# Kernel optimization log

Measured on AMD Instinct MI355X. Metric: run time of the kernel, lower is better.

## Reference

```python
import jax, jax.numpy as jnp
import numpy as np

N_NODES = 50000
N_EDGES = 800000
NODE_F = 5
EDGE_F = 4
HID = 128


def _glorot(key, shape):
    fan_in, fan_out = shape[0], shape[1]
    lim = float(np.sqrt(6.0 / (fan_in + fan_out)))
    return jax.random.uniform(key, shape, jnp.float32, -lim, lim)


def setup_inputs() -> dict:
    key = jax.random.key(0)
    ks = jax.random.split(key, 12)
    x = jax.random.normal(ks[0], (N_NODES, NODE_F), jnp.float32)
    edge_attr = jax.random.normal(ks[1], (N_EDGES, EDGE_F), jnp.float32)
    edge_index = jax.random.randint(ks[2], (2, N_EDGES), 0, N_NODES, jnp.int64)
    return {
        "x": x,
        "edge_attr": edge_attr,
        "W1": _glorot(ks[3], (NODE_F, HID)),
        "b1": jnp.zeros((HID,), jnp.float32),
        "W2": _glorot(ks[4], (HID, HID)),
        "b2": jnp.zeros((HID,), jnp.float32),
        "Wm1": _glorot(ks[5], (2 * HID + EDGE_F, HID)),
        "bm1": jnp.zeros((HID,), jnp.float32),
        "Wm2": _glorot(ks[6], (HID, 1)),
        "bm2": jnp.zeros((1,), jnp.float32),
        "edge_index": edge_index,
    }


def _gcn_conv(x, W, b, row, col, norm, n_nodes):
    # GCNConv: out = D^{-1/2} (A + I) D^{-1/2} X W + b
    xw = x @ W                                   # [N, H]
    msg = norm[:, None] * xw[row]                # [E+N, H] gather + scale
    agg = jax.ops.segment_sum(msg, col, num_segments=n_nodes)
    return agg + b


def reference(x, edge_attr, W1, b1, W2, b2, Wm1, bm1, Wm2, bm2, edge_index):
    n = x.shape[0]
    src, dst = edge_index[0], edge_index[1]
    # add self-loops (PyG GCNConv default)
    loop = jnp.arange(n, dtype=edge_index.dtype)
    row = jnp.concatenate([src, loop])
    col = jnp.concatenate([dst, loop])
    # symmetric normalization, in-degree w/ self-loops
    deg = jax.ops.segment_sum(jnp.ones_like(col, dtype=x.dtype), col, num_segments=n)
    dis = jnp.where(deg > 0, jax.lax.rsqrt(deg), 0.0)
    norm = dis[row] * dis[col]

    h = jax.nn.relu(_gcn_conv(x, W1, b1, row, col, norm, n))
    h = _gcn_conv(h, W2, b2, row, col, norm, n)

    # gather-concat edge MLP
    edge_emb = jnp.concatenate([h[src], h[dst], edge_attr], axis=1)  # [E, 2H+F]
    out = jax.nn.relu(edge_emb @ Wm1 + bm1) @ Wm2 + bm2              # [E, 1]
    return jax.nn.sigmoid(out[:, 0])
```

## Files before the change

### kernel.cpp

```cpp
#include <hip/hip_runtime.h>
#include <math.h>

#define HID 128
typedef unsigned int uint;
typedef __attribute__((ext_vector_type(8))) __bf16 bf16x8;
typedef __attribute__((ext_vector_type(4))) float f32x4;
typedef __attribute__((ext_vector_type(2))) float f32x2;


__device__ __forceinline__ uint pack_bf2(float x, float y) {
    union { float f; uint u; } a, b;
    a.f = x; b.f = y;
    uint lo = (a.u + 0x7fffu + ((a.u >> 16) & 1u)) >> 16;
    uint hi = (b.u + 0x7fffu + ((b.u >> 16) & 1u)) & 0xffff0000u;
    return lo | hi;
}

__device__ __forceinline__ unsigned short bf16r(float x) {
    union { float f; uint u; } a; a.f = x;
    return (unsigned short)((a.u + 0x7fffu + ((a.u >> 16) & 1u)) >> 16);
}

__device__ __forceinline__ f32x2 bf2f(uint v) {
    union { uint u[2]; f32x2 f; } r;
    r.u[0] = v << 16;
    r.u[1] = v & 0xffff0000u;
    return r.f;
}

__device__ __forceinline__ f32x2 mk2(float s) { f32x2 r; r.x = s; r.y = s; return r; }
__device__ __forceinline__ f32x2 max2z(f32x2 a) {
    f32x2 r; r.x = fmaxf(a.x, 0.f); r.y = fmaxf(a.y, 0.f); return r;
}

template<int CTRL>
__device__ __forceinline__ float dpp_add(float x) {
    union { float f; int i; } u, r;
    u.f = x;
    r.i = __builtin_amdgcn_update_dpp(0, u.i, CTRL, 0xf, 0xf, true);
    return x + r.f;
}


__global__ void prep_kernel(const float* __restrict__ W2, const float* __restrict__ Wm1,
                            const float* __restrict__ b2, const float* __restrict__ bm1,
                            uint* __restrict__ fWc, float* __restrict__ brow) {
    int t0 = blockIdx.x * blockDim.x + threadIdx.x;
    if (t0 < 65536) {
        int ks = t0 & 3;
        int i = t0 >> 2;
        int p = i & 3, lane = (i >> 2) & 63, kk = (i >> 8) & 3, ct = i >> 10;
        int k = kk * 32 + (lane >> 4) * 8 + p * 2;
        int n2 = ct * 16 + (lane & 15);
        const float* wmc = (n2 < 128) ? (Wm1 + n2) : (Wm1 + 128 * HID + (n2 - 128));
        const float* w2r0 = W2 + (size_t)k * HID + ks * 32;
        const float* w2r1 = w2r0 + HID;
        const float* wm = wmc + (size_t)(ks * 32) * HID;
        float d0 = 0.f, d1 = 0.f;
        #pragma unroll 8
        for (int j = 0; j < 32; ++j) {
            float w = wm[(size_t)j * HID];
            d0 += w2r0[j] * w;
            d1 += w2r1[j] * w;
        }
        d0 = dpp_add<0xB1>(d0); d0 = dpp_add<0x4E>(d0);
        d1 = dpp_add<0xB1>(d1); d1 = dpp_add<0x4E>(d1);
        if (ks == 0) fWc[i] = pack_bf2(d0, d1);
    } else if (t0 < 65536 + 1024) {
        int r = t0 - 65536;
        int ks = r & 3;
        int i = r >> 2;
        const float* wmc = (i < 128) ? (Wm1 + i) : (Wm1 + 128 * HID + (i - 128));
        float d = 0.f;
        for (int j = ks * 32; j < ks * 32 + 32; ++j) d += b2[j] * wmc[(size_t)j * HID];
        d = dpp_add<0xB1>(d); d = dpp_add<0x4E>(d);
        if (ks == 0) brow[i] = d + ((i < 128) ? bm1[i] : 0.f);
    }
}

__global__ void hist_rank(const int* __restrict__ dst, int* __restrict__ cnt,
                          int* __restrict__ rank, int E) {
    int e = blockIdx.x * blockDim.x + threadIdx.x;
    if (e < E) rank[e] = atomicAdd(&cnt[dst[e]], 1);
}

__global__ void scan1(const int* __restrict__ cnt, int* __restrict__ excl,
                      int* __restrict__ bsum, int N) {
    __shared__ int sh[256];
    int tid = threadIdx.x;
    int gid = blockIdx.x * 256 + tid;
    int v = (gid < N) ? cnt[gid] : 0;
    sh[tid] = v;
    __syncthreads();
    for (int o = 1; o < 256; o <<= 1) {
        int t = (tid >= o) ? sh[tid - o] : 0;
        __syncthreads();
        sh[tid] += t;
        __syncthreads();
    }
    if (gid < N) excl[gid] = sh[tid] - v;
    if (tid == 255) bsum[blockIdx.x] = sh[255];
}

__global__ void scan3x(const int* __restrict__ cnt, int* __restrict__ rowptr,
                       const int* __restrict__ bsum,
                       float* __restrict__ dis, const float* __restrict__ x,
                       uint4* __restrict__ xps, int N, int E, int NB) {
    __shared__ int sh[256];
    __shared__ int ex[256];
    int tid = threadIdx.x;
    int v = (tid < NB) ? bsum[tid] : 0;
    sh[tid] = v;
    __syncthreads();
    for (int o = 1; o < 256; o <<= 1) {
        int t = (tid >= o) ? sh[tid - o] : 0;
        __syncthreads();
        sh[tid] += t;
        __syncthreads();
    }
    ex[tid] = sh[tid] - v;
    __syncthreads();
    int gid = blockIdx.x * 256 + tid;
    if (gid < N) {
        rowptr[gid] = rowptr[gid] + ex[blockIdx.x];
        float dn = rsqrtf((float)cnt[gid] + 1.0f);
        dis[gid] = dn;
        const float* xr = x + (size_t)gid * 5;
        uint4 pk;
        pk.x = pack_bf2(dn * xr[0], dn * xr[1]);
        pk.y = pack_bf2(dn * xr[2], dn * xr[3]);
        pk.z = pack_bf2(dn * xr[4], 0.f);
        pk.w = 0u;
        xps[gid] = pk;
    }
    if (gid == N) rowptr[N] = E;
}

__global__ void scatter2(const int* __restrict__ src, const int* __restrict__ dst,
                         const int* __restrict__ rowptr, const int* __restrict__ rank,
                         uint2* __restrict__ csr2, int E) {
    int e = blockIdx.x * blockDim.x + threadIdx.x;
    if (e < E) {
        int d = dst[e];
        int pos = rowptr[d] + rank[e];
        csr2[pos] = make_uint2((uint)src[e] | ((uint)d << 16), (uint)e);
    }
}

__launch_bounds__(256)
__global__ void layer1_kernel(const uint4* __restrict__ xps, const uint2* __restrict__ csr2,
                              const int* __restrict__ rowptr, const float* __restrict__ dis,
                              const float* __restrict__ W1, const float* __restrict__ b1,
                              uint* __restrict__ hs1, int N) {
    __shared__ float sW[5 * HID];
    __shared__ float sb[HID];
    int tid = threadIdx.x;
    for (int i = tid; i < 5 * HID; i += 256) sW[i] = W1[i];
    for (int i = tid; i < HID; i += 256) sb[i] = b1[i];
    __syncthreads();

    int sub = tid & 3;
    int n = blockIdx.x * 64 + (tid >> 2);
    if (n >= N) return;
    int beg = rowptr[n], end = rowptr[n + 1];
    float a0 = 0.f, a1 = 0.f, a2 = 0.f, a3 = 0.f, a4 = 0.f;
    for (int i = beg + sub; i < end; i += 4) {
        uint s = csr2[i].x & 0xffffu;
        uint4 v = xps[s];
        f32x2 v01 = bf2f(v.x), v23 = bf2f(v.y), v4 = bf2f(v.z);
        a0 += v01.x; a1 += v01.y; a2 += v23.x; a3 += v23.y; a4 += v4.x;
    }
    a0 = dpp_add<0xB1>(a0); a0 = dpp_add<0x4E>(a0);
    a1 = dpp_add<0xB1>(a1); a1 = dpp_add<0x4E>(a1);
    a2 = dpp_add<0xB1>(a2); a2 = dpp_add<0x4E>(a2);
    a3 = dpp_add<0xB1>(a3); a3 = dpp_add<0x4E>(a3);
    a4 = dpp_add<0xB1>(a4); a4 = dpp_add<0x4E>(a4);
    {
        uint4 v = xps[n];
        f32x2 v01 = bf2f(v.x), v23 = bf2f(v.y), v4 = bf2f(v.z);
        a0 += v01.x; a1 += v01.y; a2 += v23.x; a3 += v23.y; a4 += v4.x;
    }
    float dn = dis[n];
    a0 *= dn; a1 *= dn; a2 *= dn; a3 *= dn; a4 *= dn;

    uint* op = hs1 + (size_t)n * 64;
    #pragma unroll
    for (int p = 0; p < 16; ++p) {
        int q = p * 4 + sub;
        int j = q * 2;
        float t0 = sb[j]     + a0 * sW[j]     + a1 * sW[HID + j]     + a2 * sW[2*HID + j]
                             + a3 * sW[3*HID + j] + a4 * sW[4*HID + j];
        float t1 = sb[j + 1] + a0 * sW[j + 1] + a1 * sW[HID + j + 1] + a2 * sW[2*HID + j + 1]
                             + a3 * sW[3*HID + j + 1] + a4 * sW[4*HID + j + 1];
        op[q] = pack_bf2(fmaxf(t0, 0.f) * dn, fmaxf(t1, 0.f) * dn);
    }
}

__launch_bounds__(256)
__global__ void agg_gemm(const uint4* __restrict__ hs1, const uint2* __restrict__ csr2,
                         const int* __restrict__ rowptr, const float* __restrict__ dis,
                         const uint4* __restrict__ Bf, const float* __restrict__ brow,
                         unsigned short* __restrict__ out, int N) {
    __shared__ uint gt[16][64];
    int wave = threadIdx.x >> 6, lane = threadIdx.x & 63;
    int gl = lane & 15, grp = lane >> 4;
    int nb = blockIdx.x * 16;
    int r0 = nb + wave * 4;

    int rp[5];
    #pragma unroll
    for (int j = 0; j < 5; ++j) {
        int idx = r0 + j;
        rp[j] = rowptr[(idx <= N) ? idx : N];
    }

    for (int q = 0; q < 4; ++q) {
        int r = wave * 4 + q;
        int n = nb + r;
        if (n < N) {
            int beg = rp[q], end = rp[q + 1];
            f32x2 acc[4];
            #pragma unroll
            for (int p = 0; p < 4; ++p) acc[p] = mk2(0.f);
            for (int base = beg + grp; base < end; base += 16) {
                int i1 = base + 4, i2 = base + 8, i3 = base + 12;
                uint s0 = csr2[base].x & 0xffffu;
                uint s1 = csr2[(i1 < end) ? i1 : beg].x & 0xffffu;
                uint s2 = csr2[(i2 < end) ? i2 : beg].x & 0xffffu;
                uint s3 = csr2[(i3 < end) ? i3 : beg].x & 0xffffu;
                uint4 v0 = hs1[(s0 << 4) + (uint)gl];
                uint4 v1 = hs1[(s1 << 4) + (uint)gl];
                uint4 v2 = hs1[(s2 << 4) + (uint)gl];
                uint4 v3 = hs1[(s3 << 4) + (uint)gl];
                f32x2 w1 = mk2((i1 < end) ? 1.f : 0.f);
                f32x2 w2 = mk2((i2 < end) ? 1.f : 0.f);
                f32x2 w3 = mk2((i3 < end) ? 1.f : 0.f);
                acc[0] += bf2f(v0.x);  acc[1] += bf2f(v0.y);
                acc[2] += bf2f(v0.z);  acc[3] += bf2f(v0.w);
                acc[0] += bf2f(v1.x) * w1;  acc[1] += bf2f(v1.y) * w1;
                acc[2] += bf2f(v1.z) * w1;  acc[3] += bf2f(v1.w) * w1;
                acc[0] += bf2f(v2.x) * w2;  acc[1] += bf2f(v2.y) * w2;
                acc[2] += bf2f(v2.z) * w2;  acc[3] += bf2f(v2.w) * w2;
                acc[0] += bf2f(v3.x) * w3;  acc[1] += bf2f(v3.y) * w3;
                acc[2] += bf2f(v3.z) * w3;  acc[3] += bf2f(v3.w) * w3;
            }
            #pragma unroll
            for (int p = 0; p < 4; ++p) {
                f32x2 t;
                t.x = __shfl_xor(acc[p].x, 16, 64); t.y = __shfl_xor(acc[p].y, 16, 64);
                acc[p] += t;
                t.x = __shfl_xor(acc[p].x, 32, 64); t.y = __shfl_xor(acc[p].y, 32, 64);
                acc[p] += t;
            }
            if (grp == 0) {
                uint4 sv = hs1[((uint)n << 4) + (uint)gl];
                f32x2 dn = mk2(dis[n]);
                f32x2 o0 = (acc[0] + bf2f(sv.x)) * dn;
                f32x2 o1 = (acc[1] + bf2f(sv.y)) * dn;
                f32x2 o2 = (acc[2] + bf2f(sv.z)) * dn;
                f32x2 o3 = (acc[3] + bf2f(sv.w)) * dn;
                gt[r][gl * 4]     = pack_bf2(o0.x, o0.y);
                gt[r][gl * 4 + 1] = pack_bf2(o1.x, o1.y);
                gt[r][gl * 4 + 2] = pack_bf2(o2.x, o2.y);
                gt[r][gl * 4 + 3] = pack_bf2(o3.x, o3.y);
            }
        } else if (grp == 0) {
            gt[r][gl * 4] = 0; gt[r][gl * 4 + 1] = 0;
            gt[r][gl * 4 + 2] = 0; gt[r][gl * 4 + 3] = 0;
        }
    }
    __syncthreads();

    int quad = lane >> 4;
    bf16x8 afr[4];
    #pragma unroll
    for (int kk = 0; kk < 4; ++kk)
        afr[kk] = *(const bf16x8*)&gt[gl][kk * 16 + quad * 4];

    for (int cc = 0; cc < 4; ++cc) {
        int c = wave * 4 + cc;
        f32x4 acc = {0.f, 0.f, 0.f, 0.f};
        #pragma unroll
        for (int kk = 0; kk < 4; ++kk) {
            bf16x8 bfr = *(const bf16x8*)&Bf[(size_t)(c * 4 + kk) * 64 + lane];
            acc = __builtin_amdgcn_mfma_f32_16x16x32_bf16(afr[kk], bfr, acc, 0, 0, 0);
        }
        float bv = brow[c * 16 + gl];
        #pragma unroll
        for (int reg = 0; reg < 4; ++reg) {
            int row = nb + quad * 4 + reg;
            if (row < N)
                out[(size_t)row * 256 + c * 16 + gl] = bf16r(acc[reg] + bv);
        }
    }
}

__launch_bounds__(256)
__global__ void edge_mlp_kernel(const uint4* __restrict__ HsHd, const float4* __restrict__ ea,
                                const uint2* __restrict__ csr2,
                                const float* __restrict__ Wb, const float* __restrict__ Wm2,
                                const float* __restrict__ bm2,
                                float* __restrict__ out, int E) {
    int lane = threadIdx.x & 63;
    int gl = lane & 15, grp = lane >> 4;

    f32x2 wb[4][4], w2[4];
    #pragma unroll
    for (int k = 0; k < 4; ++k) {
        const f32x2* wp = (const f32x2*)(Wb + k * HID + gl * 8);
        #pragma unroll
        for (int p = 0; p < 4; ++p) wb[k][p] = wp[p];
    }
    {
        const f32x2* wp = (const f32x2*)(Wm2 + gl * 8);
        #pragma unroll
        for (int p = 0; p < 4; ++p) w2[p] = wp[p];
    }
    float b2v = bm2[0];

    int gwave = (blockIdx.x * blockDim.x + threadIdx.x) >> 6;
    int nw = (gridDim.x * blockDim.x) >> 6;
    int stride = nw * 16;
    int base = gwave * 16;
    if (base >= E) return;

    uint2 ce[4];
    #pragma unroll
    for (int t = 0; t < 4; ++t) {
        int i = base + grp * 4 + t;
        ce[t] = csr2[(i < E) ? i : 0];
    }

    while (base < E) {
        int nbase = base + stride;

        uint4 hv[4], dv[4];
        float4 eav[4];
        uint eid[4];
        #pragma unroll
        for (int t = 0; t < 4; ++t) {
            uint cx = ce[t].x;
            eid[t] = ce[t].y;
            hv[t] = HsHd[((cx & 0xffffu) << 5) + (uint)gl];
            dv[t] = HsHd[((cx >> 16) << 5) + 16u + (uint)gl];
            eav[t] = ea[eid[t]];
        }

        if (nbase < E) {
            #pragma unroll
            for (int t = 0; t < 4; ++t) {
                int i = nbase + grp * 4 + t;
                ce[t] = csr2[(i < E) ? i : 0];
            }
        }

        float pr[4];
        #pragma unroll
        for (int t = 0; t < 4; ++t) {
            uint hu[4] = {hv[t].x, hv[t].y, hv[t].z, hv[t].w};
            uint du[4] = {dv[t].x, dv[t].y, dv[t].z, dv[t].w};
            f32x2 e0 = mk2(eav[t].x), e1 = mk2(eav[t].y);
            f32x2 e2 = mk2(eav[t].z), e3 = mk2(eav[t].w);
            f32x2 p2 = mk2(0.f);
            #pragma unroll
            for (int p = 0; p < 4; ++p) {
                f32x2 tt = bf2f(hu[p]) + bf2f(du[p]);
                tt += e0 * wb[0][p];
                tt += e1 * wb[1][p];
                tt += e2 * wb[2][p];
                tt += e3 * wb[3][p];
                tt = max2z(tt);
                p2 += tt * w2[p];
            }
            pr[t] = p2.x + p2.y;
        }
        #pragma unroll
        for (int t = 0; t < 4; ++t) {
            float s = pr[t];
            s = dpp_add<0xB1>(s);
            s = dpp_add<0x4E>(s);
            s = dpp_add<0x124>(s);
            s = dpp_add<0x128>(s);
            pr[t] = s;
        }
        if (gl == 0) {
            #pragma unroll
            for (int t = 0; t < 4; ++t) {
                int i = base + grp * 4 + t;
                if (i < E)
                    out[eid[t]] = 1.f / (1.f + exp2f(-1.44269504f * (pr[t] + b2v)));
            }
        }
        base = nbase;
    }
}


extern "C" void kernel_launch(void* const* d_in, const int* in_sizes, int n_in,
                              void* d_out, int out_size, void* d_ws, size_t ws_size,
                              hipStream_t stream) {
    const float* x    = (const float*)d_in[0];
    const float* ea   = (const float*)d_in[1];
    const float* W1   = (const float*)d_in[2];
    const float* b1   = (const float*)d_in[3];
    const float* W2   = (const float*)d_in[4];
    const float* b2   = (const float*)d_in[5];
    const float* Wm1  = (const float*)d_in[6];
    const float* bm1  = (const float*)d_in[7];
    const float* Wm2  = (const float*)d_in[8];
    const float* bm2  = (const float*)d_in[9];
    const int*   ei   = (const int*)d_in[10];

    const int N = in_sizes[0] / 5;
    const int E = in_sizes[1] / 4;
    const int* src = ei;
    const int* dst = ei + E;
    float* out = (float*)d_out;

    char* ws = (char*)d_ws;
    size_t off = 0;
    auto alloc = [&](size_t bytes) -> void* {
        void* p = ws + off;
        off = (off + bytes + 255) & ~(size_t)255;
        return p;
    };
    int*    cnt    = (int*)alloc((size_t)N * 4);
    int*    rowptr = (int*)alloc((size_t)(N + 1) * 4);
    int*    bsum   = (int*)alloc(256 * 4);
    float*  dis    = (float*)alloc((size_t)N * 4);
    int*    rank   = (int*)alloc((size_t)(E + 8) * 4);
    uint2*  csr2   = (uint2*)alloc((size_t)(E + 8) * 8);
    uint4*  xps    = (uint4*)alloc((size_t)N * 16);
    uint*   hs1    = (uint*)alloc((size_t)N * 64 * 4);
    uint*   HsHd   = (uint*)alloc((size_t)N * 128 * 4);
    uint*   fWc    = (uint*)alloc(16384 * 4);
    float*  brow   = (float*)alloc(256 * 4);
    (void)ws_size; (void)n_in; (void)out_size;

    const int NB = (N + 255) / 256;
    const int EB = (E + 255) / 256;

    hipMemsetAsync(cnt, 0, (size_t)N * 4, stream);
    prep_kernel<<<260, 256, 0, stream>>>(W2, Wm1, b2, bm1, fWc, brow);
    hist_rank<<<EB, 256, 0, stream>>>(dst, cnt, rank, E);
    scan1<<<NB, 256, 0, stream>>>(cnt, rowptr, bsum, N);
    scan3x<<<NB, 256, 0, stream>>>(cnt, rowptr, bsum, dis, x, xps, N, E, NB);
    scatter2<<<EB, 256, 0, stream>>>(src, dst, rowptr, rank, csr2, E);

    layer1_kernel<<<(N + 63) / 64, 256, 0, stream>>>(xps, csr2, rowptr, dis, W1, b1, hs1, N);

    agg_gemm<<<(N + 15) / 16, 256, 0, stream>>>((const uint4*)hs1, csr2, rowptr, dis,
                                                (const uint4*)fWc, brow,
                                                (unsigned short*)HsHd, N);

    edge_mlp_kernel<<<2048, 256, 0, stream>>>((const uint4*)HsHd, (const float4*)ea, csr2,
                                              Wm1 + 256 * HID, Wm2, bm2, out, E);
}
```

Before: 252.5 us.

## Aggregate layer-2 with MFMA one-hot matmul and make edge MLP node-centric

The layer-2 neighbor aggregation now stages 32-edge chunks of source rows into LDS and sums them with bf16 MFMA using a one-hot ownership matrix, replacing per-row scalar accumulation. The self loop is folded in as a final chunk. The edge MLP now assigns one 16-lane group per destination node, so the destination half of the hidden state is loaded once and reused across that node's edges, and it uses packed-FP32 inline asm. Edge attributes are also permuted into CSR order during scatter so the edge MLP reads them contiguously, at the cost of an extra workspace buffer and an extra write in scatter.

```diff
diff --git a/kernel.cpp b/kernel.cpp
--- a/kernel.cpp
+++ b/kernel.cpp
@@ -3,6 +3,8 @@
 
 #define HID 128
 typedef unsigned int uint;
+typedef unsigned short u16;
+typedef unsigned char u8;
 typedef __attribute__((ext_vector_type(8))) __bf16 bf16x8;
 typedef __attribute__((ext_vector_type(4))) float f32x4;
 typedef __attribute__((ext_vector_type(2))) float f32x2;
@@ -39,6 +41,17 @@
     u.f = x;
     r.i = __builtin_amdgcn_update_dpp(0, u.i, CTRL, 0xf, 0xf, true);
     return x + r.f;
+}
+
+__device__ __forceinline__ f32x2 pk_add2(f32x2 a, f32x2 b) {
+    f32x2 d;
+    asm("v_pk_add_f32 %0, %1, %2" : "=v"(d) : "v"(a), "v"(b));
+    return d;
+}
+__device__ __forceinline__ f32x2 pk_fma2(f32x2 a, f32x2 b, f32x2 c) {
+    f32x2 d;
+    asm("v_pk_fma_f32 %0, %1, %2, %3" : "=v"(d) : "v"(a), "v"(b), "v"(c));
+    return d;
 }
 
 
@@ -138,12 +151,15 @@
 
 __global__ void scatter2(const int* __restrict__ src, const int* __restrict__ dst,
                          const int* __restrict__ rowptr, const int* __restrict__ rank,
-                         uint2* __restrict__ csr2, int E) {
+                         const float4* __restrict__ ea,
+                         uint2* __restrict__ csr2, float4* __restrict__ ear,
+                         int use_ear, int E) {
     int e = blockIdx.x * blockDim.x + threadIdx.x;
     if (e < E) {
         int d = dst[e];
         int pos = rowptr[d] + rank[e];
         csr2[pos] = make_uint2((uint)src[e] | ((uint)d << 16), (uint)e);
+        if (use_ear) ear[pos] = ea[e];
     }
 }
 
@@ -201,108 +217,121 @@
                          const int* __restrict__ rowptr, const float* __restrict__ dis,
                          const uint4* __restrict__ Bf, const float* __restrict__ brow,
                          unsigned short* __restrict__ out, int N) {
-    __shared__ uint gt[16][64];
-    int wave = threadIdx.x >> 6, lane = threadIdx.x & 63;
-    int gl = lane & 15, grp = lane >> 4;
+    __shared__ u16 Bs[32 * 128];
+    __shared__ u16 gtu[16 * 128];
+    __shared__ u16 ssrc[32];
+    __shared__ __align__(8) u8 sown[32];
+
+    int tid = threadIdx.x;
+    int wave = tid >> 6, lane = tid & 63;
+    int gl = lane & 15, q = lane >> 4;
     int nb = blockIdx.x * 16;
-    int r0 = nb + wave * 4;
-
-    int rp[5];
+
+    int hi = nb + 16; if (hi > N) hi = N;
+    int e0 = rowptr[nb];
+    int e1 = rowptr[hi];
+    int nchunk = (e1 - e0 + 31) >> 5;
+
+    f32x4 acc0 = {0.f, 0.f, 0.f, 0.f};
+    f32x4 acc1 = {0.f, 0.f, 0.f, 0.f};
+    int colb0 = (wave * 2) * 16 + gl;
+    int colb1 = (wave * 2 + 1) * 16 + gl;
+
+    for (int c = 0; c <= nchunk; ++c) {
+        if (tid < 32) {
+            uint own = 0xffu, sid = (uint)nb;
+            if (c < nchunk) {
+                int i = e0 + c * 32 + tid;
+                if (i < e1) {
+                    uint cx = csr2[i].x;
+                    sid = cx & 0xffffu;
+                    own = (cx >> 16) - (uint)nb;
+                }
+            } else if (tid < 16 && nb + tid < N) {
+                own = (uint)tid; sid = (uint)(nb + tid);
+            }
+            ssrc[tid] = (u16)sid;
+            sown[tid] = (u8)own;
+        }
+        __syncthreads();
+        #pragma unroll
+        for (int p = 0; p < 2; ++p) {
+            int idx = tid + p * 256;
+            int slot = idx >> 4, cu = idx & 15;
+            uint sid = (uint)ssrc[slot];
+            uint4 v = hs1[(size_t)sid * 16 + cu];
+            *(uint4*)((char*)Bs + ((idx * 16) ^ ((slot >> 3) << 4))) = v;
+        }
+        __syncthreads();
+        uint2 ob = *(const uint2*)&sown[q * 8];
+        union { uint u[4]; bf16x8 v; } au;
+        #pragma unroll
+        for (int pj = 0; pj < 4; ++pj) {
+            uint bsrc = (pj < 2) ? ob.x : ob.y;
+            uint sh = (uint)(pj & 1) * 16u;
+            uint o0 = (bsrc >> sh) & 0xffu;
+            uint o1 = (bsrc >> (sh + 8u)) & 0xffu;
+            au.u[pj] = ((o0 == (uint)gl) ? 0x3f80u : 0u) |
+                       ((o1 == (uint)gl) ? 0x3f800000u : 0u);
+        }
+        union { u16 s[8]; bf16x8 v; } b0u, b1u;
+        int sw = q << 4;
+        #pragma unroll
+        for (int j = 0; j < 8; ++j) {
+            int k = q * 8 + j;
+            b0u.s[j] = *(const u16*)((const char*)Bs + (((k * 128 + colb0) * 2) ^ sw));
+            b1u.s[j] = *(const u16*)((const char*)Bs + (((k * 128 + colb1) * 2) ^ sw));
+        }
+        acc0 = __builtin_amdgcn_mfma_f32_16x16x32_bf16(au.v, b0u.v, acc0, 0, 0, 0);
+        acc1 = __builtin_amdgcn_mfma_f32_16x16x32_bf16(au.v, b1u.v, acc1, 0, 0, 0);
+        __syncthreads();
+    }
+
     #pragma unroll
-    for (int j = 0; j < 5; ++j) {
-        int idx = r0 + j;
-        rp[j] = rowptr[(idx <= N) ? idx : N];
-    }
-
-    for (int q = 0; q < 4; ++q) {
-        int r = wave * 4 + q;
+    for (int reg = 0; reg < 4; ++reg) {
+        int r = q * 4 + reg;
         int n = nb + r;
-        if (n < N) {
-            int beg = rp[q], end = rp[q + 1];
-            f32x2 acc[4];
-            #pragma unroll
-            for (int p = 0; p < 4; ++p) acc[p] = mk2(0.f);
-            for (int base = beg + grp; base < end; base += 16) {
-                int i1 = base + 4, i2 = base + 8, i3 = base + 12;
-                uint s0 = csr2[base].x & 0xffffu;
-                uint s1 = csr2[(i1 < end) ? i1 : beg].x & 0xffffu;
-                uint s2 = csr2[(i2 < end) ? i2 : beg].x & 0xffffu;
-                uint s3 = csr2[(i3 < end) ? i3 : beg].x & 0xffffu;
-                uint4 v0 = hs1[(s0 << 4) + (uint)gl];
-                uint4 v1 = hs1[(s1 << 4) + (uint)gl];
-                uint4 v2 = hs1[(s2 << 4) + (uint)gl];
-                uint4 v3 = hs1[(s3 << 4) + (uint)gl];
-                f32x2 w1 = mk2((i1 < end) ? 1.f : 0.f);
-                f32x2 w2 = mk2((i2 < end) ? 1.f : 0.f);
-                f32x2 w3 = mk2((i3 < end) ? 1.f : 0.f);
-                acc[0] += bf2f(v0.x);  acc[1] += bf2f(v0.y);
-                acc[2] += bf2f(v0.z);  acc[3] += bf2f(v0.w);
-                acc[0] += bf2f(v1.x) * w1;  acc[1] += bf2f(v1.y) * w1;
-                acc[2] += bf2f(v1.z) * w1;  acc[3] += bf2f(v1.w) * w1;
-                acc[0] += bf2f(v2.x) * w2;  acc[1] += bf2f(v2.y) * w2;
-                acc[2] += bf2f(v2.z) * w2;  acc[3] += bf2f(v2.w) * w2;
-                acc[0] += bf2f(v3.x) * w3;  acc[1] += bf2f(v3.y) * w3;
-                acc[2] += bf2f(v3.z) * w3;  acc[3] += bf2f(v3.w) * w3;
-            }
-            #pragma unroll
-            for (int p = 0; p < 4; ++p) {
-                f32x2 t;
-                t.x = __shfl_xor(acc[p].x, 16, 64); t.y = __shfl_xor(acc[p].y, 16, 64);
-                acc[p] += t;
-                t.x = __shfl_xor(acc[p].x, 32, 64); t.y = __shfl_xor(acc[p].y, 32, 64);
-                acc[p] += t;
-            }
-            if (grp == 0) {
-                uint4 sv = hs1[((uint)n << 4) + (uint)gl];
-                f32x2 dn = mk2(dis[n]);
-                f32x2 o0 = (acc[0] + bf2f(sv.x)) * dn;
-                f32x2 o1 = (acc[1] + bf2f(sv.y)) * dn;
-                f32x2 o2 = (acc[2] + bf2f(sv.z)) * dn;
-                f32x2 o3 = (acc[3] + bf2f(sv.w)) * dn;
-                gt[r][gl * 4]     = pack_bf2(o0.x, o0.y);
-                gt[r][gl * 4 + 1] = pack_bf2(o1.x, o1.y);
-                gt[r][gl * 4 + 2] = pack_bf2(o2.x, o2.y);
-                gt[r][gl * 4 + 3] = pack_bf2(o3.x, o3.y);
-            }
-        } else if (grp == 0) {
-            gt[r][gl * 4] = 0; gt[r][gl * 4 + 1] = 0;
-            gt[r][gl * 4 + 2] = 0; gt[r][gl * 4 + 3] = 0;
-        }
+        float dn = (n < N) ? dis[n] : 0.f;
+        gtu[r * 128 + colb0] = bf16r(acc0[reg] * dn);
+        gtu[r * 128 + colb1] = bf16r(acc1[reg] * dn);
     }
     __syncthreads();
 
-    int quad = lane >> 4;
+    uint* gtp = (uint*)gtu;
     bf16x8 afr[4];
     #pragma unroll
     for (int kk = 0; kk < 4; ++kk)
-        afr[kk] = *(const bf16x8*)&gt[gl][kk * 16 + quad * 4];
+        afr[kk] = *(const bf16x8*)&gtp[gl * 64 + kk * 16 + q * 4];
 
     for (int cc = 0; cc < 4; ++cc) {
-        int c = wave * 4 + cc;
-        f32x4 acc = {0.f, 0.f, 0.f, 0.f};
+        int cC = wave * 4 + cc;
+        f32x4 a2 = {0.f, 0.f, 0.f, 0.f};
         #pragma unroll
         for (int kk = 0; kk < 4; ++kk) {
-            bf16x8 bfr = *(const bf16x8*)&Bf[(size_t)(c * 4 + kk) * 64 + lane];
-            acc = __builtin_amdgcn_mfma_f32_16x16x32_bf16(afr[kk], bfr, acc, 0, 0, 0);
-        }
-        float bv = brow[c * 16 + gl];
+            bf16x8 bfr = *(const bf16x8*)&Bf[(size_t)(cC * 4 + kk) * 64 + lane];
+            a2 = __builtin_amdgcn_mfma_f32_16x16x32_bf16(afr[kk], bfr, a2, 0, 0, 0);
+        }
+        float bv = brow[cC * 16 + gl];
         #pragma unroll
         for (int reg = 0; reg < 4; ++reg) {
-            int row = nb + quad * 4 + reg;
+            int row = nb + q * 4 + reg;
             if (row < N)
-                out[(size_t)row * 256 + c * 16 + gl] = bf16r(acc[reg] + bv);
+                out[(size_t)row * 256 + cC * 16 + gl] = bf16r(a2[reg] + bv);
         }
     }
 }
 
 __launch_bounds__(256)
-__global__ void edge_mlp_kernel(const uint4* __restrict__ HsHd, const float4* __restrict__ ea,
+__global__ void edge_mlp_kernel(const uint4* __restrict__ HsHd,
+                                const float4* __restrict__ ea,
+                                const float4* __restrict__ ear, int use_ear,
                                 const uint2* __restrict__ csr2,
+                                const int* __restrict__ rowptr,
                                 const float* __restrict__ Wb, const float* __restrict__ Wm2,
                                 const float* __restrict__ bm2,
-                                float* __restrict__ out, int E) {
+                                float* __restrict__ out, int N) {
     int lane = threadIdx.x & 63;
-    int gl = lane & 15, grp = lane >> 4;
+    int gl = lane & 15;
 
     f32x2 wb[4][4], w2[4];
     #pragma unroll
@@ -318,59 +347,42 @@
     }
     float b2v = bm2[0];
 
-    int gwave = (blockIdx.x * blockDim.x + threadIdx.x) >> 6;
-    int nw = (gridDim.x * blockDim.x) >> 6;
-    int stride = nw * 16;
-    int base = gwave * 16;
-    if (base >= E) return;
-
-    uint2 ce[4];
-    #pragma unroll
-    for (int t = 0; t < 4; ++t) {
-        int i = base + grp * 4 + t;
-        ce[t] = csr2[(i < E) ? i : 0];
-    }
-
-    while (base < E) {
-        int nbase = base + stride;
-
-        uint4 hv[4], dv[4];
+    int n = (int)((blockIdx.x * 256u + threadIdx.x) >> 4);
+    if (n >= N) return;
+    int beg = rowptr[n], end = rowptr[n + 1];
+    if (beg >= end) return;
+
+    uint4 dvv = HsHd[(size_t)n * 32 + 16 + gl];
+    f32x2 hd[4] = {bf2f(dvv.x), bf2f(dvv.y), bf2f(dvv.z), bf2f(dvv.w)};
+
+    for (int base = beg; base < end; base += 4) {
+        uint2 ce[4];
+        uint4 hv[4];
         float4 eav[4];
-        uint eid[4];
         #pragma unroll
         for (int t = 0; t < 4; ++t) {
-            uint cx = ce[t].x;
-            eid[t] = ce[t].y;
-            hv[t] = HsHd[((cx & 0xffffu) << 5) + (uint)gl];
-            dv[t] = HsHd[((cx >> 16) << 5) + 16u + (uint)gl];
-            eav[t] = ea[eid[t]];
-        }
-
-        if (nbase < E) {
-            #pragma unroll
-            for (int t = 0; t < 4; ++t) {
-                int i = nbase + grp * 4 + t;
-                ce[t] = csr2[(i < E) ? i : 0];
-            }
-        }
-
+            int i = base + t;
+            int j = (i < end) ? i : beg;
+            ce[t] = csr2[j];
+            hv[t] = HsHd[(size_t)((ce[t].x & 0xffffu) << 5) + gl];
+            eav[t] = use_ear ? ear[j] : ea[ce[t].y];
+        }
         float pr[4];
         #pragma unroll
         for (int t = 0; t < 4; ++t) {
             uint hu[4] = {hv[t].x, hv[t].y, hv[t].z, hv[t].w};
-            uint du[4] = {dv[t].x, dv[t].y, dv[t].z, dv[t].w};
             f32x2 e0 = mk2(eav[t].x), e1 = mk2(eav[t].y);
             f32x2 e2 = mk2(eav[t].z), e3 = mk2(eav[t].w);
             f32x2 p2 = mk2(0.f);
             #pragma unroll
             for (int p = 0; p < 4; ++p) {
-                f32x2 tt = bf2f(hu[p]) + bf2f(du[p]);
-                tt += e0 * wb[0][p];
-                tt += e1 * wb[1][p];
-                tt += e2 * wb[2][p];
-                tt += e3 * wb[3][p];
+                f32x2 tt = pk_add2(bf2f(hu[p]), hd[p]);
+                tt = pk_fma2(e0, wb[0][p], tt);
+                tt = pk_fma2(e1, wb[1][p], tt);
+                tt = pk_fma2(e2, wb[2][p], tt);
+                tt = pk_fma2(e3, wb[3][p], tt);
                 tt = max2z(tt);
-                p2 += tt * w2[p];
+                p2 = pk_fma2(tt, w2[p], p2);
             }
             pr[t] = p2.x + p2.y;
         }
@@ -386,12 +398,11 @@
         if (gl == 0) {
             #pragma unroll
             for (int t = 0; t < 4; ++t) {
-                int i = base + grp * 4 + t;
-                if (i < E)
-                    out[eid[t]] = 1.f / (1.f + exp2f(-1.44269504f * (pr[t] + b2v)));
+                int i = base + t;
+                if (i < end)
+                    out[ce[t].y] = 1.f / (1.f + exp2f(-1.44269504f * (pr[t] + b2v)));
             }
         }
-        base = nbase;
     }
 }
 
@@ -435,7 +446,9 @@
     uint*   HsHd   = (uint*)alloc((size_t)N * 128 * 4);
     uint*   fWc    = (uint*)alloc(16384 * 4);
     float*  brow   = (float*)alloc(256 * 4);
-    (void)ws_size; (void)n_in; (void)out_size;
+    float4* ear    = (float4*)alloc((size_t)(E + 8) * 16);
+    int use_ear = (off <= ws_size) ? 1 : 0;
+    (void)n_in; (void)out_size;
 
     const int NB = (N + 255) / 256;
     const int EB = (E + 255) / 256;
@@ -445,7 +458,8 @@
     hist_rank<<<EB, 256, 0, stream>>>(dst, cnt, rank, E);
     scan1<<<NB, 256, 0, stream>>>(cnt, rowptr, bsum, N);
     scan3x<<<NB, 256, 0, stream>>>(cnt, rowptr, bsum, dis, x, xps, N, E, NB);
-    scatter2<<<EB, 256, 0, stream>>>(src, dst, rowptr, rank, csr2, E);
+    scatter2<<<EB, 256, 0, stream>>>(src, dst, rowptr, rank, (const float4*)ea,
+                                     csr2, ear, use_ear, E);
 
     layer1_kernel<<<(N + 63) / 64, 256, 0, stream>>>(xps, csr2, rowptr, dis, W1, b1, hs1, N);
 
@@ -453,6 +467,8 @@
                                                 (const uint4*)fWc, brow,
                                                 (unsigned short*)HsHd, N);
 
-    edge_mlp_kernel<<<2048, 256, 0, stream>>>((const uint4*)HsHd, (const float4*)ea, csr2,
-                                              Wm1 + 256 * HID, Wm2, bm2, out, E);
-}
+    edge_mlp_kernel<<<(N + 15) / 16, 256, 0, stream>>>((const uint4*)HsHd,
+                                                       (const float4*)ea, (const float4*)ear,
+                                                       use_ear, csr2, rowptr,
+                                                       Wm1 + 256 * HID, Wm2, bm2, out, N);
+}
```

New measurement: 269.0 us. 6.5% more time.
